# Kernel tuning notes

Measured on AMD Instinct MI355X. Metric: run time of the kernel, lower is better.

## Reference

```python
import jax, jax.numpy as jnp
import numpy as np

INPUT_SIZE = 21
HIDDEN = 50
OUTPUT = 24
BATCH = 4096
SEQ = 336


def setup_inputs() -> dict:
    key = jax.random.key(0)
    ks = jax.random.split(key, 7)
    s_ih = 1.0 / np.sqrt(HIDDEN)
    x = jax.random.normal(ks[0], (BATCH, SEQ, INPUT_SIZE), dtype=jnp.float32)
    # PyTorch LSTM params: gate order i, f, g, o stacked along dim0
    W_ih = jax.random.uniform(ks[1], (4 * HIDDEN, INPUT_SIZE), minval=-s_ih, maxval=s_ih, dtype=jnp.float32)
    W_hh = jax.random.uniform(ks[2], (4 * HIDDEN, HIDDEN), minval=-s_ih, maxval=s_ih, dtype=jnp.float32)
    b_ih = jax.random.uniform(ks[3], (4 * HIDDEN,), minval=-s_ih, maxval=s_ih, dtype=jnp.float32)
    b_hh = jax.random.uniform(ks[4], (4 * HIDDEN,), minval=-s_ih, maxval=s_ih, dtype=jnp.float32)
    s_fc = 1.0 / np.sqrt(HIDDEN)
    W_fc = jax.random.uniform(ks[5], (OUTPUT, HIDDEN), minval=-s_fc, maxval=s_fc, dtype=jnp.float32)
    b_fc = jax.random.uniform(ks[6], (OUTPUT,), minval=-s_fc, maxval=s_fc, dtype=jnp.float32)
    return {"x": x, "W_ih": W_ih, "W_hh": W_hh, "b_ih": b_ih, "b_hh": b_hh, "W_fc": W_fc, "b_fc": b_fc}


def _lstm_last(x, W_ih, W_hh, b_ih, b_hh):
    B = x.shape[0]
    H = W_hh.shape[1]
    # Precompute input projections for all timesteps: [T, B, 4H]
    x_proj = jnp.einsum('bti,gi->tbg', x, W_ih) + (b_ih + b_hh)

    def step(carry, xp):
        h, c = carry
        gates = xp + h @ W_hh.T  # [B, 4H]
        i_g, f_g, g_g, o_g = jnp.split(gates, 4, axis=-1)
        i_g = jax.nn.sigmoid(i_g)
        f_g = jax.nn.sigmoid(f_g)
        g_g = jnp.tanh(g_g)
        o_g = jax.nn.sigmoid(o_g)
        c = f_g * c + i_g * g_g
        h = o_g * jnp.tanh(c)
        return (h, c), None

    h0 = jnp.zeros((B, H), dtype=x.dtype)
    c0 = jnp.zeros((B, H), dtype=x.dtype)
    (h_last, _), _ = jax.lax.scan(step, (h0, c0), x_proj)
    return h_last


def reference(x, W_ih, W_hh, b_ih, b_hh, W_fc, b_fc):
    h_last = _lstm_last(x, W_ih, W_hh, b_ih, b_hh)  # [B, H]
    return h_last @ W_fc.T + b_fc  # [B, OUTPUT]
```

## Files before the change

### kernel.cpp

```cpp
#include <hip/hip_runtime.h>


#define T_SEQ 336
#define I_IN  21
#define HID   50
#define O_OUT 24
#define MB    16
#define NT    512
#define TPW   2
#define CH    12
#define NCH   28
#define XELEM (CH * MB * I_IN)
#define NLD   8
#define XBUFH (CH * 4 * 16 * 8)

#define HIDX(buf, kb, n, j) ((((buf)*8 + (kb))*16 + (n))*8 + (j))
#define XIDX(s, kb, n, j)   ((((s)*4 + (kb))*16 + (n))*8 + (j))

#define K_LOG2E 1.44269504088896340736f

typedef _Float16 f16x8 __attribute__((ext_vector_type(8)));
typedef float    f32x4 __attribute__((ext_vector_type(4)));

static __device__ __forceinline__ float frcp(float v) { return __builtin_amdgcn_rcpf(v); }
static __device__ __forceinline__ float ex2(float v)  { return __builtin_amdgcn_exp2f(v); }
static __device__ __forceinline__ float sigm2(float g) { return frcp(1.f + ex2(g)); }
static __device__ __forceinline__ float tanh2(float g) {
    return __builtin_fmaf(-2.f, frcp(1.f + ex2(g)), 1.f);
}

__global__ __launch_bounds__(NT)
void lstm_mfma9(const float* __restrict__ x,
                const float* __restrict__ W_ih,
                const float* __restrict__ W_hh,
                const float* __restrict__ b_ih,
                const float* __restrict__ b_hh,
                const float* __restrict__ W_fc,
                const float* __restrict__ b_fc,
                float* __restrict__ out)
{
    __shared__ _Float16 hbuf[2 * 8 * 16 * 8];
    __shared__ _Float16 xC[2 * XBUFH];

    const int tid  = threadIdx.x;
    const int lane = tid & 63;
    const int wv   = tid >> 6;
    const int nl   = lane & 15;
    const int q    = lane >> 4;
    const int b0   = blockIdx.x * MB;

    for (int i = tid; i < 2 * 8 * 16 * 8; i += NT) hbuf[i] = (_Float16)0.f;
    for (int i = tid; i < 2 * XBUFH;      i += NT) xC[i]   = (_Float16)0.f;

    const float* px[NLD];
    int  xdst[NLD];
    bool xv[NLD];
    float sv[NLD];
    #pragma unroll
    for (int k = 0; k < NLD; ++k) {
        const int e  = tid + k * NT;
        const int i  = e % I_IN;
        const int r  = e / I_IN;
        const int b  = r & 15;
        const int sI = r >> 4;
        xv[k]   = (e < XELEM);
        px[k]   = x + ((size_t)(b0 + b) * T_SEQ + sI) * I_IN + i;
        xdst[k] = XIDX(sI, i >> 3, b, i & 7);
        sv[k]   = px[k][0];
    }

    f16x8 Wh[TPW][3], Wl[TPW][3];
    f32x4 biasv[TPW];
    #pragma unroll
    for (int tt = 0; tt < TPW; ++tt) {
        const int t    = wv * TPW + tt;
        const int p    = t * 16 + nl;
        const int unit = p >> 2, gate = p & 3;
        const bool vr  = (unit < HID);
        const float ws = (gate == 2) ? (2.f * K_LOG2E) : (-K_LOG2E);
        const int orig = gate * HID + unit;
        const int ub   = t * 4 + q;
        #pragma unroll
        for (int r = 0; r < 4; ++r) {
            const float bs = (r == 2) ? (2.f * K_LOG2E) : (-K_LOG2E);
            biasv[tt][r] = (ub < HID) ? (b_ih[r * HID + ub] + b_hh[r * HID + ub]) * bs : 0.f;
        }
        #pragma unroll
        for (int kc = 0; kc < 3; ++kc) {
            #pragma unroll
            for (int j = 0; j < 8; ++j) {
                const int k = kc * 32 + q * 8 + j;
                float w = 0.f;
                if (vr) {
                    if (k < 64) { if (k < HID) w = W_hh[orig * HID + k]; }
                    else { const int ki = k - 64; if (ki < I_IN) w = W_ih[orig * I_IN + ki]; }
                }
                w *= ws;
                const _Float16 hi = (_Float16)w;
                Wh[tt][kc][j] = hi;
                Wl[tt][kc][j] = (_Float16)(w - (float)hi);
            }
        }
    }

    __syncthreads();

    #pragma unroll
    for (int k = 0; k < NLD; ++k) {
        if (xv[k]) xC[xdst[k]] = (_Float16)sv[k];
        px[k] += CH * I_IN;
    }

    const int u0 = (wv * TPW + 0) * 4 + q;
    const int u1 = (wv * TPW + 1) * 4 + q;
    const int hwo0 = ((u0 >> 3) * 16 + nl) * 8 + (u0 & 7);
    const int hwo1 = ((u1 >> 3) * 16 + nl) * 8 + (u1 & 7);
    float cst0 = 0.f, cst1 = 0.f;

    const _Float16* hb0 = &hbuf[HIDX(0, q, nl, 0)];
    const int bfo = ((q * 16) + nl) * 8;

    for (int c = 0; c < NCH; ++c) {
        const int  rb    = (c & 1) * XBUFH;
        const int  wb    = ((c + 1) & 1) * XBUFH;
        const bool dostg = (c + 1) < NCH;
        #pragma unroll 2
        for (int s = 0; s < CH; ++s) {
            __syncthreads();

            if (s == 0 && dostg) {
                #pragma unroll
                for (int k = 0; k < NLD; ++k) sv[k] = px[k][0];
            }

            const int cur = s & 1, nxt = cur ^ 1;

            const _Float16* hb = hb0 + cur * 1024;
            const f16x8 B0 = *(const f16x8*)(hb);
            const f16x8 B1 = *(const f16x8*)(hb + 4 * 16 * 8);
            const f16x8 B2 = *(const f16x8*)&xC[rb + s * 512 + bfo];

            f32x4 aA0 = biasv[0];
            f32x4 aB0 = {0.f, 0.f, 0.f, 0.f};
            f32x4 aA1 = biasv[1];
            f32x4 aB1 = {0.f, 0.f, 0.f, 0.f};
            aA0 = __builtin_amdgcn_mfma_f32_16x16x32_f16(Wh[0][0], B0, aA0, 0, 0, 0);
            aA1 = __builtin_amdgcn_mfma_f32_16x16x32_f16(Wh[1][0], B0, aA1, 0, 0, 0);
            aB0 = __builtin_amdgcn_mfma_f32_16x16x32_f16(Wl[0][0], B0, aB0, 0, 0, 0);
            aB1 = __builtin_amdgcn_mfma_f32_16x16x32_f16(Wl[1][0], B0, aB1, 0, 0, 0);
            aA0 = __builtin_amdgcn_mfma_f32_16x16x32_f16(Wh[0][1], B1, aA0, 0, 0, 0);
            aA1 = __builtin_amdgcn_mfma_f32_16x16x32_f16(Wh[1][1], B1, aA1, 0, 0, 0);
            aB0 = __builtin_amdgcn_mfma_f32_16x16x32_f16(Wl[0][1], B1, aB0, 0, 0, 0);
            aB1 = __builtin_amdgcn_mfma_f32_16x16x32_f16(Wl[1][1], B1, aB1, 0, 0, 0);
            aA0 = __builtin_amdgcn_mfma_f32_16x16x32_f16(Wh[0][2], B2, aA0, 0, 0, 0);
            aA1 = __builtin_amdgcn_mfma_f32_16x16x32_f16(Wh[1][2], B2, aA1, 0, 0, 0);
            aB0 = __builtin_amdgcn_mfma_f32_16x16x32_f16(Wl[0][2], B2, aB0, 0, 0, 0);
            aB1 = __builtin_amdgcn_mfma_f32_16x16x32_f16(Wl[1][2], B2, aB1, 0, 0, 0);

            {
                const float gi = aA0[0] + aB0[0];
                const float gf = aA0[1] + aB0[1];
                const float gg = aA0[2] + aB0[2];
                const float go = aA0[3] + aB0[3];
                const float cc = __builtin_fmaf(sigm2(gf), cst0, sigm2(gi) * tanh2(gg));
                cst0 = cc;
                const float h = sigm2(go) * tanh2(2.f * K_LOG2E * cc);
                hbuf[nxt * 1024 + hwo0] = (_Float16)h;
            }
            {
                const float gi = aA1[0] + aB1[0];
                const float gf = aA1[1] + aB1[1];
                const float gg = aA1[2] + aB1[2];
                const float go = aA1[3] + aB1[3];
                const float cc = __builtin_fmaf(sigm2(gf), cst1, sigm2(gi) * tanh2(gg));
                cst1 = cc;
                const float h = sigm2(go) * tanh2(2.f * K_LOG2E * cc);
                hbuf[nxt * 1024 + hwo1] = (_Float16)h;
            }

            if (s == 0 && dostg) {
                #pragma unroll
                for (int k = 0; k < NLD; ++k) {
                    if (xv[k]) xC[wb + xdst[k]] = (_Float16)sv[k];
                    px[k] += CH * I_IN;
                }
            }
        }
    }

    __syncthreads();
    if (tid < MB * O_OUT) {
        const int b = tid / O_OUT, o = tid % O_OUT;
        float a = b_fc[o];
        for (int u = 0; u < HID; ++u) {
            const float hv = (float)hbuf[HIDX(0, u >> 3, b, u & 7)];
            a = __builtin_fmaf(hv, W_fc[o * HID + u], a);
        }
        out[(size_t)(b0 + b) * O_OUT + o] = a;
    }
}

extern "C" void kernel_launch(void* const* d_in, const int* in_sizes, int n_in,
                              void* d_out, int out_size, void* d_ws, size_t ws_size,
                              hipStream_t stream)
{
    const float* x    = (const float*)d_in[0];
    const float* W_ih = (const float*)d_in[1];
    const float* W_hh = (const float*)d_in[2];
    const float* b_ih = (const float*)d_in[3];
    const float* b_hh = (const float*)d_in[4];
    const float* W_fc = (const float*)d_in[5];
    const float* b_fc = (const float*)d_in[6];
    float* out = (float*)d_out;

    lstm_mfma9<<<dim3(4096 / MB), dim3(NT), 0, stream>>>(
        x, W_ih, W_hh, b_ih, b_hh, W_fc, b_fc, out);
}
```

Before: 321.2 us.

## Precompute input projections one chunk ahead, off the recurrent critical path

Input-projection MFMAs for the next chunk of timesteps are computed a chunk ahead into register accumulators (xp). Each recurrent step then only runs the W_hh MFMAs, seeded with the precomputed projection, as one serial accumulation chain. Chunk size drops from 12 to 8 steps, and the step loop is fully unrolled so xp can be indexed statically. This shortens the per-step dependent chain but raises register pressure, and the hi/lo MFMAs now chain serially rather than running as independent accumulators.

```diff
diff --git a/kernel.cpp b/kernel.cpp
--- a/kernel.cpp
+++ b/kernel.cpp
@@ -8,10 +8,10 @@
 #define MB    16
 #define NT    512
 #define TPW   2
-#define CH    12
-#define NCH   28
+#define CH    8
+#define NCH   42
 #define XELEM (CH * MB * I_IN)
-#define NLD   8
+#define NLD   6
 #define XBUFH (CH * 4 * 16 * 8)
 
 #define HIDX(buf, kb, n, j) ((((buf)*8 + (kb))*16 + (n))*8 + (j))
@@ -21,6 +21,8 @@
 
 typedef _Float16 f16x8 __attribute__((ext_vector_type(8)));
 typedef float    f32x4 __attribute__((ext_vector_type(4)));
+
+#define MFMA16(A, B, C) __builtin_amdgcn_mfma_f32_16x16x32_f16((A), (B), (C), 0, 0, 0)
 
 static __device__ __forceinline__ float frcp(float v) { return __builtin_amdgcn_rcpf(v); }
 static __device__ __forceinline__ float ex2(float v)  { return __builtin_amdgcn_exp2f(v); }
@@ -30,14 +32,14 @@
 }
 
 __global__ __launch_bounds__(NT)
-void lstm_mfma9(const float* __restrict__ x,
-                const float* __restrict__ W_ih,
-                const float* __restrict__ W_hh,
-                const float* __restrict__ b_ih,
-                const float* __restrict__ b_hh,
-                const float* __restrict__ W_fc,
-                const float* __restrict__ b_fc,
-                float* __restrict__ out)
+void lstm_mfma10(const float* __restrict__ x,
+                 const float* __restrict__ W_ih,
+                 const float* __restrict__ W_hh,
+                 const float* __restrict__ b_ih,
+                 const float* __restrict__ b_hh,
+                 const float* __restrict__ W_fc,
+                 const float* __restrict__ b_fc,
+                 float* __restrict__ out)
 {
     __shared__ _Float16 hbuf[2 * 8 * 16 * 8];
     __shared__ _Float16 xC[2 * XBUFH];
@@ -62,14 +64,16 @@
         const int i  = e % I_IN;
         const int r  = e / I_IN;
         const int b  = r & 15;
-        const int sI = r >> 4;
+        const int sIr = r >> 4;
+        const int sI = (sIr < CH) ? sIr : 0;
         xv[k]   = (e < XELEM);
         px[k]   = x + ((size_t)(b0 + b) * T_SEQ + sI) * I_IN + i;
         xdst[k] = XIDX(sI, i >> 3, b, i & 7);
         sv[k]   = px[k][0];
     }
 
-    f16x8 Wh[TPW][3], Wl[TPW][3];
+    f16x8 Wh[TPW][2], Wl[TPW][2];
+    f16x8 Xh[TPW],    Xl[TPW];
     f32x4 biasv[TPW];
     #pragma unroll
     for (int tt = 0; tt < TPW; ++tt) {
@@ -86,21 +90,24 @@
             biasv[tt][r] = (ub < HID) ? (b_ih[r * HID + ub] + b_hh[r * HID + ub]) * bs : 0.f;
         }
         #pragma unroll
-        for (int kc = 0; kc < 3; ++kc) {
+        for (int kc = 0; kc < 2; ++kc) {
             #pragma unroll
             for (int j = 0; j < 8; ++j) {
                 const int k = kc * 32 + q * 8 + j;
-                float w = 0.f;
-                if (vr) {
-                    if (k < 64) { if (k < HID) w = W_hh[orig * HID + k]; }
-                    else { const int ki = k - 64; if (ki < I_IN) w = W_ih[orig * I_IN + ki]; }
-                }
-                w *= ws;
+                const float w = (vr && k < HID) ? W_hh[orig * HID + k] * ws : 0.f;
                 const _Float16 hi = (_Float16)w;
                 Wh[tt][kc][j] = hi;
                 Wl[tt][kc][j] = (_Float16)(w - (float)hi);
             }
         }
+        #pragma unroll
+        for (int j = 0; j < 8; ++j) {
+            const int k = q * 8 + j;
+            const float w = (vr && k < I_IN) ? W_ih[orig * I_IN + k] * ws : 0.f;
+            const _Float16 hi = (_Float16)w;
+            Xh[tt][j] = hi;
+            Xl[tt][j] = (_Float16)(w - (float)hi);
+        }
     }
 
     __syncthreads();
@@ -110,6 +117,7 @@
         if (xv[k]) xC[xdst[k]] = (_Float16)sv[k];
         px[k] += CH * I_IN;
     }
+    __syncthreads();
 
     const int u0 = (wv * TPW + 0) * 4 + q;
     const int u1 = (wv * TPW + 1) * 4 + q;
@@ -120,11 +128,21 @@
     const _Float16* hb0 = &hbuf[HIDX(0, q, nl, 0)];
     const int bfo = ((q * 16) + nl) * 8;
 
+    f32x4 xp[TPW][CH];
+    #pragma unroll
+    for (int s = 0; s < CH; ++s) {
+        const f16x8 XN = *(const f16x8*)&xC[s * 512 + bfo];
+        xp[0][s] = MFMA16(Xh[0], XN, biasv[0]);
+        xp[0][s] = MFMA16(Xl[0], XN, xp[0][s]);
+        xp[1][s] = MFMA16(Xh[1], XN, biasv[1]);
+        xp[1][s] = MFMA16(Xl[1], XN, xp[1][s]);
+    }
+
     for (int c = 0; c < NCH; ++c) {
         const int  rb    = (c & 1) * XBUFH;
         const int  wb    = ((c + 1) & 1) * XBUFH;
         const bool dostg = (c + 1) < NCH;
-        #pragma unroll 2
+        #pragma unroll
         for (int s = 0; s < CH; ++s) {
             __syncthreads();
 
@@ -137,44 +155,48 @@
 
             const _Float16* hb = hb0 + cur * 1024;
             const f16x8 B0 = *(const f16x8*)(hb);
-            const f16x8 B1 = *(const f16x8*)(hb + 4 * 16 * 8);
-            const f16x8 B2 = *(const f16x8*)&xC[rb + s * 512 + bfo];
-
-            f32x4 aA0 = biasv[0];
-            f32x4 aB0 = {0.f, 0.f, 0.f, 0.f};
-            f32x4 aA1 = biasv[1];
-            f32x4 aB1 = {0.f, 0.f, 0.f, 0.f};
-            aA0 = __builtin_amdgcn_mfma_f32_16x16x32_f16(Wh[0][0], B0, aA0, 0, 0, 0);
-            aA1 = __builtin_amdgcn_mfma_f32_16x16x32_f16(Wh[1][0], B0, aA1, 0, 0, 0);
-            aB0 = __builtin_amdgcn_mfma_f32_16x16x32_f16(Wl[0][0], B0, aB0, 0, 0, 0);
-            aB1 = __builtin_amdgcn_mfma_f32_16x16x32_f16(Wl[1][0], B0, aB1, 0, 0, 0);
-            aA0 = __builtin_amdgcn_mfma_f32_16x16x32_f16(Wh[0][1], B1, aA0, 0, 0, 0);
-            aA1 = __builtin_amdgcn_mfma_f32_16x16x32_f16(Wh[1][1], B1, aA1, 0, 0, 0);
-            aB0 = __builtin_amdgcn_mfma_f32_16x16x32_f16(Wl[0][1], B1, aB0, 0, 0, 0);
-            aB1 = __builtin_amdgcn_mfma_f32_16x16x32_f16(Wl[1][1], B1, aB1, 0, 0, 0);
-            aA0 = __builtin_amdgcn_mfma_f32_16x16x32_f16(Wh[0][2], B2, aA0, 0, 0, 0);
-            aA1 = __builtin_amdgcn_mfma_f32_16x16x32_f16(Wh[1][2], B2, aA1, 0, 0, 0);
-            aB0 = __builtin_amdgcn_mfma_f32_16x16x32_f16(Wl[0][2], B2, aB0, 0, 0, 0);
-            aB1 = __builtin_amdgcn_mfma_f32_16x16x32_f16(Wl[1][2], B2, aB1, 0, 0, 0);
+            const f16x8 B1 = *(const f16x8*)(hb + 512);
+
+            f32x4 a0 = xp[0][s];
+            f32x4 a1 = xp[1][s];
+            a0 = MFMA16(Wh[0][0], B0, a0);
+            a1 = MFMA16(Wh[1][0], B0, a1);
+            a0 = MFMA16(Wh[0][1], B1, a0);
+            a1 = MFMA16(Wh[1][1], B1, a1);
+            a0 = MFMA16(Wl[0][0], B0, a0);
+            a1 = MFMA16(Wl[1][0], B0, a1);
+            a0 = MFMA16(Wl[0][1], B1, a0);
+            a1 = MFMA16(Wl[1][1], B1, a1);
+
+            if (dostg && s >= 1) {
+                const int sp = s - 1;
+                const f16x8 XN = *(const f16x8*)&xC[wb + sp * 512 + bfo];
+                xp[0][sp] = MFMA16(Xh[0], XN, biasv[0]);
+                xp[0][sp] = MFMA16(Xl[0], XN, xp[0][sp]);
+                xp[1][sp] = MFMA16(Xh[1], XN, biasv[1]);
+                xp[1][sp] = MFMA16(Xl[1], XN, xp[1][sp]);
+            }
+            if (dostg && s == CH - 1) {
+                const int sp = CH - 1;
+                const f16x8 XN = *(const f16x8*)&xC[wb + sp * 512 + bfo];
+                xp[0][sp] = MFMA16(Xh[0], XN, biasv[0]);
+                xp[0][sp] = MFMA16(Xl[0], XN, xp[0][sp]);
+                xp[1][sp] = MFMA16(Xh[1], XN, biasv[1]);
+                xp[1][sp] = MFMA16(Xl[1], XN, xp[1][sp]);
+            }
 
             {
-                const float gi = aA0[0] + aB0[0];
-                const float gf = aA0[1] + aB0[1];
-                const float gg = aA0[2] + aB0[2];
-                const float go = aA0[3] + aB0[3];
-                const float cc = __builtin_fmaf(sigm2(gf), cst0, sigm2(gi) * tanh2(gg));
+                const float cc = __builtin_fmaf(sigm2(a0[1]), cst0,
+                                                sigm2(a0[0]) * tanh2(a0[2]));
                 cst0 = cc;
-                const float h = sigm2(go) * tanh2(2.f * K_LOG2E * cc);
+                const float h = sigm2(a0[3]) * tanh2(2.f * K_LOG2E * cc);
                 hbuf[nxt * 1024 + hwo0] = (_Float16)h;
             }
             {
-                const float gi = aA1[0] + aB1[0];
-                const float gf = aA1[1] + aB1[1];
-                const float gg = aA1[2] + aB1[2];
-                const float go = aA1[3] + aB1[3];
-                const float cc = __builtin_fmaf(sigm2(gf), cst1, sigm2(gi) * tanh2(gg));
+                const float cc = __builtin_fmaf(sigm2(a1[1]), cst1,
+                                                sigm2(a1[0]) * tanh2(a1[2]));
                 cst1 = cc;
-                const float h = sigm2(go) * tanh2(2.f * K_LOG2E * cc);
+                const float h = sigm2(a1[3]) * tanh2(2.f * K_LOG2E * cc);
                 hbuf[nxt * 1024 + hwo1] = (_Float16)h;
             }
 
@@ -213,6 +235,6 @@
     const float* b_fc = (const float*)d_in[6];
     float* out = (float*)d_out;
 
-    lstm_mfma9<<<dim3(4096 / MB), dim3(NT), 0, stream>>>(
+    lstm_mfma10<<<dim3(4096 / MB), dim3(NT), 0, stream>>>(
         x, W_ih, W_hh, b_ih, b_hh, W_fc, b_fc, out);
 }
```

Result: slower. 333.1 us (+3.7%).
